# Kernel optimization log

Measured on AMD Instinct MI355X. Metric: run time of the kernel, lower is better.

The kernel has to match this reference:

```python
import jax, jax.numpy as jnp
import numpy as np
from jax.scipy.special import logsumexp

B, N, D, H = 8, 2048, 3, 256
BLUR = 0.001            # geomloss blur
EPS0 = 32.0             # ~diameter^2/2 for unit-std gaussian clouds
N_ITERS = 14            # eps-scaling steps down to blur^2
EPS_LIST = np.geomspace(EPS0, BLUR ** 2, N_ITERS).astype(np.float32)


def _sqdist(x, y):
    # x: [B,N,3], y: [B,M,3] -> [B,N,M] squared euclidean distance
    x2 = jnp.sum(x * x, -1)[:, :, None]
    y2 = jnp.sum(y * y, -1)[:, None, :]
    xy = jnp.einsum('bnd,bmd->bnm', x, y)
    return jnp.maximum(x2 + y2 - 2.0 * xy, 0.0)


def sinkhorn_potential_g(x, y):
    """Log-domain Sinkhorn (p=2 cost ||x-y||^2/2, uniform weights) with
    epsilon scaling; returns second dual potential g over y. Mimics
    geomloss.SamplesLoss('sinkhorn', p=2, blur=0.001, potentials=True)."""
    C = 0.5 * _sqdist(x, y)                      # [B,N,M]
    n, m = x.shape[1], y.shape[1]
    loga = -jnp.log(jnp.float32(n))
    logb = -jnp.log(jnp.float32(m))
    f = jnp.zeros((x.shape[0], n), C.dtype)
    g = jnp.zeros((x.shape[0], m), C.dtype)
    for eps in EPS_LIST:
        f = -eps * logsumexp(logb + (g[:, None, :] - C) / eps, axis=2)
        g = -eps * logsumexp(loga + (f[:, :, None] - C) / eps, axis=1)
    return g


def get_hard_assignment(x, y):
    # idx such that y[idx] is the OT match for x
    g = sinkhorn_potential_g(x, y)                       # [B,M]
    C_minus_g = _sqdist(x, y) - g[:, None, :]            # [B,N,M]
    return jnp.argmin(C_minus_g, axis=2)                 # [B,N]


def setup_inputs() -> dict:
    key = jax.random.key(0)
    ks = jax.random.split(key, 8)
    return {
        'cloud': jax.random.normal(ks[0], (B, N, D), jnp.float32),
        'noise': jax.random.normal(ks[1], (B, N, D), jnp.float32),
        't': jax.random.uniform(ks[2], (B,), jnp.float32),
        'W1': jax.random.normal(ks[3], (D, H), jnp.float32) * 0.1,
        'Wt': jax.random.normal(ks[4], (H,), jnp.float32) * 0.1,
        'b1': jnp.zeros((H,), jnp.float32),
        'W2': jax.random.normal(ks[5], (H, D), jnp.float32) * 0.1,
        'b2': jnp.zeros((D,), jnp.float32),
    }


def reference(cloud, noise, t, W1, Wt, b1, W2, b2):
    # std normalization (torch.std -> unbiased, ddof=1), done under no_grad
    std = jnp.std(cloud, axis=(1, 2), keepdims=True, ddof=1)
    x0 = cloud / std
    idx = get_hard_assignment(noise, x0)                 # [B,N] int
    x0_aligned = jnp.take_along_axis(x0, idx[:, :, None], axis=1)  # [B,N,3]
    tv = t[:, None, None]
    x_t = (1.0 - tv) * x0_aligned + tv * noise
    # stand-in diffusion network: per-point MLP conditioned on t
    h = jax.nn.relu(jnp.einsum('bnd,dh->bnh', x_t, W1) + tv * Wt + b1)
    v_pred = jnp.einsum('bnh,hd->bnd', h, W2) + b2
    v = noise - x0_aligned
    return v_pred, v
```

## Files before the change

### kernel.cpp

```cpp
#include <hip/hip_runtime.h>
#include <math.h>

#define B_ 8
#define N_ 2048
#define D_ 3
#define H_ 256
#define ND_ (N_*D_)
#define BN_ (B_*N_)

__global__ __launch_bounds__(256) void std_kernel(const float* __restrict__ cloud,
                                                  float* __restrict__ stdv) {
  __shared__ float red[256];
  int b = blockIdx.x, tid = threadIdx.x;
  const float* p = cloud + (size_t)b * ND_;
  float s = 0.f;
  for (int i = tid; i < ND_; i += 256) s += p[i];
  red[tid] = s; __syncthreads();
  for (int off = 128; off > 0; off >>= 1) {
    if (tid < off) red[tid] += red[tid + off];
    __syncthreads();
  }
  float mean = red[0] / (float)ND_;
  __syncthreads();
  float ss = 0.f;
  for (int i = tid; i < ND_; i += 256) { float d = p[i] - mean; ss += d * d; }
  red[tid] = ss; __syncthreads();
  for (int off = 128; off > 0; off >>= 1) {
    if (tid < off) red[tid] += red[tid + off];
    __syncthreads();
  }
  if (tid == 0) stdv[b] = sqrtf(red[0] / (float)(ND_ - 1));
}

__global__ __launch_bounds__(256) void prep_kernel(const float* __restrict__ cloud,
    const float* __restrict__ noise, const float* __restrict__ stdv,
    float4* __restrict__ x0p, float4* __restrict__ np4,
    float* __restrict__ f, float* __restrict__ g) {
  int i = blockIdx.x * 256 + threadIdx.x;
  if (i >= BN_) return;
  int b = i >> 11;
  float sd = stdv[b];
  float cx = cloud[3*i] / sd, cy = cloud[3*i+1] / sd, cz = cloud[3*i+2] / sd;
  x0p[i] = make_float4(cx, cy, cz, cx*cx + cy*cy + cz*cz);
  float ax = noise[3*i], ay = noise[3*i+1], az = noise[3*i+2];
  np4[i] = make_float4(ax, ay, az, ax*ax + ay*ay + az*az);
  f[i] = 0.f; g[i] = 0.f;
}

__global__ __launch_bounds__(256, 2) void lse_kernel(
    const float4* __restrict__ outer, const float4* __restrict__ inner,
    const float* __restrict__ pin, float* __restrict__ pout,
    float scl, float kk, float hh, float c1, float c2) {
  __shared__ float4 sP[N_];
  int tid = threadIdx.x;
  int b = blockIdx.x >> 7;
  int rowBase = (blockIdx.x & 127) << 4;
  int base = b * N_;
  for (int j = tid; j < N_; j += 256) {
    float4 p = inner[base + j];
    float q = kk * pin[base + j] - hh * p.w;
    sP[j] = make_float4(scl * p.x, scl * p.y, scl * p.z, q);
  }
  __syncthreads();
  int wave = tid >> 6, lane = tid & 63;
  int r0 = base + rowBase + (wave << 2);
  float4 A0 = outer[r0], A1 = outer[r0+1], A2 = outer[r0+2], A3 = outer[r0+3];
  float a0x = scl*A0.x, a0y = scl*A0.y, a0z = scl*A0.z, rc0 = -hh*A0.w;
  float a1x = scl*A1.x, a1y = scl*A1.y, a1z = scl*A1.z, rc1 = -hh*A1.w;
  float a2x = scl*A2.x, a2y = scl*A2.y, a2z = scl*A2.z, rc2 = -hh*A2.w;
  float a3x = scl*A3.x, a3y = scl*A3.y, a3z = scl*A3.z, rc3 = -hh*A3.w;
  float v0[32], v1[32], v2[32], v3[32];
  float m0 = -INFINITY, m1 = -INFINITY, m2 = -INFINITY, m3 = -INFINITY;
#pragma unroll
  for (int jj = 0; jj < 32; ++jj) {
    float4 p = sP[(jj << 6) + lane];
    float t0 = fmaf(p.x, a0x, p.w); t0 = fmaf(p.y, a0y, t0); t0 = fmaf(p.z, a0z, t0);
    v0[jj] = t0; m0 = fmaxf(m0, t0);
    float t1 = fmaf(p.x, a1x, p.w); t1 = fmaf(p.y, a1y, t1); t1 = fmaf(p.z, a1z, t1);
    v1[jj] = t1; m1 = fmaxf(m1, t1);
    float t2 = fmaf(p.x, a2x, p.w); t2 = fmaf(p.y, a2y, t2); t2 = fmaf(p.z, a2z, t2);
    v2[jj] = t2; m2 = fmaxf(m2, t2);
    float t3 = fmaf(p.x, a3x, p.w); t3 = fmaf(p.y, a3y, t3); t3 = fmaf(p.z, a3z, t3);
    v3[jj] = t3; m3 = fmaxf(m3, t3);
  }
#pragma unroll
  for (int off = 32; off >= 1; off >>= 1) {
    m0 = fmaxf(m0, __shfl_xor(m0, off, 64));
    m1 = fmaxf(m1, __shfl_xor(m1, off, 64));
    m2 = fmaxf(m2, __shfl_xor(m2, off, 64));
    m3 = fmaxf(m3, __shfl_xor(m3, off, 64));
  }
  float s0 = 0.f, s1 = 0.f, s2 = 0.f, s3 = 0.f;
#pragma unroll
  for (int jj = 0; jj < 32; ++jj) {
    s0 += __builtin_amdgcn_exp2f(v0[jj] - m0);
    s1 += __builtin_amdgcn_exp2f(v1[jj] - m1);
    s2 += __builtin_amdgcn_exp2f(v2[jj] - m2);
    s3 += __builtin_amdgcn_exp2f(v3[jj] - m3);
  }
#pragma unroll
  for (int off = 32; off >= 1; off >>= 1) {
    s0 += __shfl_xor(s0, off, 64);
    s1 += __shfl_xor(s1, off, 64);
    s2 += __shfl_xor(s2, off, 64);
    s3 += __shfl_xor(s3, off, 64);
  }
  if (lane == 0) {
    pout[r0]   = fmaf(c1, rc0 + m0 + __builtin_amdgcn_logf(s0), c2);
    pout[r0+1] = fmaf(c1, rc1 + m1 + __builtin_amdgcn_logf(s1), c2);
    pout[r0+2] = fmaf(c1, rc2 + m2 + __builtin_amdgcn_logf(s2), c2);
    pout[r0+3] = fmaf(c1, rc3 + m3 + __builtin_amdgcn_logf(s3), c2);
  }
}

__global__ __launch_bounds__(256) void assign_mlp_kernel(
    const float4* __restrict__ np4, const float4* __restrict__ x0p,
    const float* __restrict__ g, const float* __restrict__ t,
    const float* __restrict__ W1, const float* __restrict__ Wt,
    const float* __restrict__ b1, const float* __restrict__ W2,
    const float* __restrict__ b2, float* __restrict__ out) {
  __shared__ float4 sPts[N_];
  __shared__ float  sg[N_];
  __shared__ float  sW1[3*H_], sWt[H_], sb1[H_], sW2[H_*3], sb2[3];
  int tid = threadIdx.x;
  int b = blockIdx.x >> 8;
  int rowBase = (blockIdx.x & 255) << 3;
  int base = b * N_;
  for (int j = tid; j < N_; j += 256) { sPts[j] = x0p[base+j]; sg[j] = g[base+j]; }
  for (int i = tid; i < 3*H_; i += 256) { sW1[i] = W1[i]; sW2[i] = W2[i]; }
  if (tid < H_) { sWt[tid] = Wt[tid]; sb1[tid] = b1[tid]; }
  if (tid < 3) sb2[tid] = b2[tid];
  __syncthreads();
  int wave = tid >> 6, lane = tid & 63;
  float tb = t[b];
  for (int rr = 0; rr < 2; ++rr) {
    int r = rowBase + (wave << 1) + rr;
    float4 A = np4[base + r];
    float best = INFINITY; int bidx = 0;
#pragma unroll
    for (int jj = 0; jj < 32; ++jj) {
      int j = (jj << 6) + lane;
      float4 p = sPts[j];
      float d = A.x*p.x + A.y*p.y + A.z*p.z;
      float val = fmaxf(A.w + p.w - 2.0f*d, 0.0f) - sg[j];
      if (val < best) { best = val; bidx = j; }
    }
#pragma unroll
    for (int off = 32; off >= 1; off >>= 1) {
      float ov = __shfl_xor(best, off, 64);
      int   oi = __shfl_xor(bidx, off, 64);
      if (ov < best || (ov == best && oi < bidx)) { best = ov; bidx = oi; }
    }
    float4 xa = sPts[bidx];
    float xtx = (1.0f - tb)*xa.x + tb*A.x;
    float xty = (1.0f - tb)*xa.y + tb*A.y;
    float xtz = (1.0f - tb)*xa.z + tb*A.z;
    float acc0 = 0.f, acc1 = 0.f, acc2 = 0.f;
#pragma unroll
    for (int hh = 0; hh < 4; ++hh) {
      int h = (hh << 6) + lane;
      float hv = xtx*sW1[h] + xty*sW1[H_+h] + xtz*sW1[2*H_+h] + tb*sWt[h] + sb1[h];
      hv = fmaxf(hv, 0.0f);
      acc0 += hv * sW2[3*h];
      acc1 += hv * sW2[3*h+1];
      acc2 += hv * sW2[3*h+2];
    }
#pragma unroll
    for (int off = 32; off >= 1; off >>= 1) {
      acc0 += __shfl_xor(acc0, off, 64);
      acc1 += __shfl_xor(acc1, off, 64);
      acc2 += __shfl_xor(acc2, off, 64);
    }
    if (lane == 0) {
      int gi = base + r;
      out[3*gi]   = acc0 + sb2[0];
      out[3*gi+1] = acc1 + sb2[1];
      out[3*gi+2] = acc2 + sb2[2];
      out[3*BN_ + 3*gi]   = A.x - xa.x;
      out[3*BN_ + 3*gi+1] = A.y - xa.y;
      out[3*BN_ + 3*gi+2] = A.z - xa.z;
    }
  }
}

extern "C" void kernel_launch(void* const* d_in, const int* in_sizes, int n_in,
                              void* d_out, int out_size, void* d_ws, size_t ws_size,
                              hipStream_t stream) {
  (void)in_sizes; (void)n_in; (void)out_size; (void)ws_size;
  const float* cloud = (const float*)d_in[0];
  const float* noise = (const float*)d_in[1];
  const float* t     = (const float*)d_in[2];
  const float* W1    = (const float*)d_in[3];
  const float* Wt    = (const float*)d_in[4];
  const float* b1    = (const float*)d_in[5];
  const float* W2    = (const float*)d_in[6];
  const float* b2w   = (const float*)d_in[7];
  float* out = (float*)d_out;

  float* ws   = (float*)d_ws;
  float* stdv = ws;
  float4* x0p = (float4*)(ws + 16);
  float4* np4 = (float4*)(ws + 16 + 4*BN_);
  float* f    = ws + 16 + 8*BN_;
  float* g    = f + BN_;

  std_kernel<<<B_, 256, 0, stream>>>(cloud, stdv);
  prep_kernel<<<BN_/256, 256, 0, stream>>>(cloud, noise, stdv, x0p, np4, f, g);

  const double LOG2E = 1.4426950408889634074;
  const double LN2   = 0.6931471805599453094;
  const double logw  = -log(2048.0);
  const double l0 = log10(32.0), l1 = log10(1e-6);
  for (int kit = 0; kit < 14; ++kit) {
    double epsd = pow(10.0, l0 + (l1 - l0) * ((double)kit / 13.0));
    float eps = (float)epsd;
    float kk  = (float)(LOG2E / (double)eps);
    float hh  = 0.5f * kk;
    float scl = sqrtf(kk);
    float c1  = (float)(-(double)eps * LN2);
    float c2  = (float)(-(double)eps * logw);
    lse_kernel<<<B_*(N_/16), 256, 0, stream>>>(np4, x0p, g, f, scl, kk, hh, c1, c2);
    lse_kernel<<<B_*(N_/16), 256, 0, stream>>>(x0p, np4, f, g, scl, kk, hh, c1, c2);
  }

  assign_mlp_kernel<<<B_*(N_/8), 256, 0, stream>>>(np4, x0p, g, t, W1, Wt, b1, W2, b2w, out);
}
```

Baseline: 415.9 us.

## Fuse all Sinkhorn iterations into one persistent kernel with per-batch grid barriers

Replaces the 28 separate log-sum-exp launches with a single persistent kernel of 256 blocks (32 per batch). Blocks synchronise through atomic counter/generation barriers between half-iterations, and the per-iteration epsilon constants are passed in as a table. This removes launch overhead and inter-kernel gaps. In exchange each block handles 64 rows instead of 16, so there are fewer blocks than before, and correctness depends on all 256 blocks being co-resident on the device.

```diff
diff --git a/kernel.cpp b/kernel.cpp
--- a/kernel.cpp
+++ b/kernel.cpp
@@ -7,6 +7,11 @@
 #define H_ 256
 #define ND_ (N_*D_)
 #define BN_ (B_*N_)
+#define NITER_ 14
+
+struct EpsTab { float scl[NITER_], kk[NITER_], hh[NITER_], c1[NITER_], c2[NITER_]; };
+
+__device__ unsigned g_bar[256];
 
 __global__ __launch_bounds__(256) void std_kernel(const float* __restrict__ cloud,
                                                   float* __restrict__ stdv) {
@@ -37,6 +42,8 @@
     float4* __restrict__ x0p, float4* __restrict__ np4,
     float* __restrict__ f, float* __restrict__ g) {
   int i = blockIdx.x * 256 + threadIdx.x;
+  if (blockIdx.x == 0)
+    __hip_atomic_store(&g_bar[threadIdx.x], 0u, __ATOMIC_RELAXED, __HIP_MEMORY_SCOPE_AGENT);
   if (i >= BN_) return;
   int b = i >> 11;
   float sd = stdv[b];
@@ -47,69 +54,108 @@
   f[i] = 0.f; g[i] = 0.f;
 }
 
-__global__ __launch_bounds__(256, 2) void lse_kernel(
-    const float4* __restrict__ outer, const float4* __restrict__ inner,
-    const float* __restrict__ pin, float* __restrict__ pout,
-    float scl, float kk, float hh, float c1, float c2) {
+__device__ inline void batch_barrier(unsigned* cnt, unsigned* gen, unsigned epoch) {
+  __syncthreads();
+  if (threadIdx.x == 0) {
+    __threadfence();
+    unsigned old = __hip_atomic_fetch_add(cnt, 1u, __ATOMIC_ACQ_REL, __HIP_MEMORY_SCOPE_AGENT);
+    if (old == 31u) {
+      __hip_atomic_store(cnt, 0u, __ATOMIC_RELAXED, __HIP_MEMORY_SCOPE_AGENT);
+      __hip_atomic_fetch_add(gen, 1u, __ATOMIC_ACQ_REL, __HIP_MEMORY_SCOPE_AGENT);
+    } else {
+      while (__hip_atomic_load(gen, __ATOMIC_ACQUIRE, __HIP_MEMORY_SCOPE_AGENT) < epoch) {
+        __builtin_amdgcn_s_sleep(2);
+      }
+    }
+    __threadfence();
+  }
+  __syncthreads();
+}
+
+__global__ __launch_bounds__(256, 2) void sinkhorn_kernel(
+    const float4* __restrict__ x0p, const float4* __restrict__ np4,
+    float* f, float* g, EpsTab tab) {
   __shared__ float4 sP[N_];
   int tid = threadIdx.x;
-  int b = blockIdx.x >> 7;
-  int rowBase = (blockIdx.x & 127) << 4;
+  int b   = blockIdx.x >> 5;
+  int blk = blockIdx.x & 31;
   int base = b * N_;
-  for (int j = tid; j < N_; j += 256) {
-    float4 p = inner[base + j];
-    float q = kk * pin[base + j] - hh * p.w;
-    sP[j] = make_float4(scl * p.x, scl * p.y, scl * p.z, q);
-  }
-  __syncthreads();
+  unsigned* cnt = &g_bar[b * 16];
+  unsigned* gen = &g_bar[128 + b * 16];
   int wave = tid >> 6, lane = tid & 63;
-  int r0 = base + rowBase + (wave << 2);
-  float4 A0 = outer[r0], A1 = outer[r0+1], A2 = outer[r0+2], A3 = outer[r0+3];
-  float a0x = scl*A0.x, a0y = scl*A0.y, a0z = scl*A0.z, rc0 = -hh*A0.w;
-  float a1x = scl*A1.x, a1y = scl*A1.y, a1z = scl*A1.z, rc1 = -hh*A1.w;
-  float a2x = scl*A2.x, a2y = scl*A2.y, a2z = scl*A2.z, rc2 = -hh*A2.w;
-  float a3x = scl*A3.x, a3y = scl*A3.y, a3z = scl*A3.z, rc3 = -hh*A3.w;
-  float v0[32], v1[32], v2[32], v3[32];
-  float m0 = -INFINITY, m1 = -INFINITY, m2 = -INFINITY, m3 = -INFINITY;
-#pragma unroll
-  for (int jj = 0; jj < 32; ++jj) {
-    float4 p = sP[(jj << 6) + lane];
-    float t0 = fmaf(p.x, a0x, p.w); t0 = fmaf(p.y, a0y, t0); t0 = fmaf(p.z, a0z, t0);
-    v0[jj] = t0; m0 = fmaxf(m0, t0);
-    float t1 = fmaf(p.x, a1x, p.w); t1 = fmaf(p.y, a1y, t1); t1 = fmaf(p.z, a1z, t1);
-    v1[jj] = t1; m1 = fmaxf(m1, t1);
-    float t2 = fmaf(p.x, a2x, p.w); t2 = fmaf(p.y, a2y, t2); t2 = fmaf(p.z, a2z, t2);
-    v2[jj] = t2; m2 = fmaxf(m2, t2);
-    float t3 = fmaf(p.x, a3x, p.w); t3 = fmaf(p.y, a3y, t3); t3 = fmaf(p.z, a3z, t3);
-    v3[jj] = t3; m3 = fmaxf(m3, t3);
-  }
-#pragma unroll
-  for (int off = 32; off >= 1; off >>= 1) {
-    m0 = fmaxf(m0, __shfl_xor(m0, off, 64));
-    m1 = fmaxf(m1, __shfl_xor(m1, off, 64));
-    m2 = fmaxf(m2, __shfl_xor(m2, off, 64));
-    m3 = fmaxf(m3, __shfl_xor(m3, off, 64));
-  }
-  float s0 = 0.f, s1 = 0.f, s2 = 0.f, s3 = 0.f;
-#pragma unroll
-  for (int jj = 0; jj < 32; ++jj) {
-    s0 += __builtin_amdgcn_exp2f(v0[jj] - m0);
-    s1 += __builtin_amdgcn_exp2f(v1[jj] - m1);
-    s2 += __builtin_amdgcn_exp2f(v2[jj] - m2);
-    s3 += __builtin_amdgcn_exp2f(v3[jj] - m3);
-  }
-#pragma unroll
-  for (int off = 32; off >= 1; off >>= 1) {
-    s0 += __shfl_xor(s0, off, 64);
-    s1 += __shfl_xor(s1, off, 64);
-    s2 += __shfl_xor(s2, off, 64);
-    s3 += __shfl_xor(s3, off, 64);
-  }
-  if (lane == 0) {
-    pout[r0]   = fmaf(c1, rc0 + m0 + __builtin_amdgcn_logf(s0), c2);
-    pout[r0+1] = fmaf(c1, rc1 + m1 + __builtin_amdgcn_logf(s1), c2);
-    pout[r0+2] = fmaf(c1, rc2 + m2 + __builtin_amdgcn_logf(s2), c2);
-    pout[r0+3] = fmaf(c1, rc3 + m3 + __builtin_amdgcn_logf(s3), c2);
+  unsigned epoch = 0;
+  for (int kit = 0; kit < NITER_; ++kit) {
+    float scl = tab.scl[kit], kk = tab.kk[kit], hh = tab.hh[kit];
+    float c1 = tab.c1[kit], c2 = tab.c2[kit];
+    for (int half = 0; half < 2; ++half) {
+      const float4* outer = half ? x0p : np4;
+      const float4* inner = half ? np4 : x0p;
+      float*        pin   = half ? f : g;
+      float*        pout  = half ? g : f;
+      for (int j = tid; j < N_; j += 256) {
+        float4 p = inner[base + j];
+        float pot = __hip_atomic_load(&pin[base + j], __ATOMIC_RELAXED, __HIP_MEMORY_SCOPE_AGENT);
+        float q = fmaf(kk, pot, -hh * p.w);
+        sP[j] = make_float4(scl * p.x, scl * p.y, scl * p.z, q);
+      }
+      __syncthreads();
+      for (int grp = 0; grp < 4; ++grp) {
+        int r0 = base + (blk << 6) + (grp << 4) + (wave << 2);
+        float4 A0 = outer[r0], A1 = outer[r0+1], A2 = outer[r0+2], A3 = outer[r0+3];
+        float a0x = scl*A0.x, a0y = scl*A0.y, a0z = scl*A0.z, rc0 = -hh*A0.w;
+        float a1x = scl*A1.x, a1y = scl*A1.y, a1z = scl*A1.z, rc1 = -hh*A1.w;
+        float a2x = scl*A2.x, a2y = scl*A2.y, a2z = scl*A2.z, rc2 = -hh*A2.w;
+        float a3x = scl*A3.x, a3y = scl*A3.y, a3z = scl*A3.z, rc3 = -hh*A3.w;
+        float v0[32], v1[32], v2[32], v3[32];
+        float m0 = -INFINITY, m1 = -INFINITY, m2 = -INFINITY, m3 = -INFINITY;
+#pragma unroll
+        for (int jj = 0; jj < 32; ++jj) {
+          float4 p = sP[(jj << 6) + lane];
+          float t0 = fmaf(p.x, a0x, p.w); t0 = fmaf(p.y, a0y, t0); t0 = fmaf(p.z, a0z, t0);
+          v0[jj] = t0; m0 = fmaxf(m0, t0);
+          float t1 = fmaf(p.x, a1x, p.w); t1 = fmaf(p.y, a1y, t1); t1 = fmaf(p.z, a1z, t1);
+          v1[jj] = t1; m1 = fmaxf(m1, t1);
+          float t2 = fmaf(p.x, a2x, p.w); t2 = fmaf(p.y, a2y, t2); t2 = fmaf(p.z, a2z, t2);
+          v2[jj] = t2; m2 = fmaxf(m2, t2);
+          float t3 = fmaf(p.x, a3x, p.w); t3 = fmaf(p.y, a3y, t3); t3 = fmaf(p.z, a3z, t3);
+          v3[jj] = t3; m3 = fmaxf(m3, t3);
+        }
+#pragma unroll
+        for (int off = 32; off >= 1; off >>= 1) {
+          m0 = fmaxf(m0, __shfl_xor(m0, off, 64));
+          m1 = fmaxf(m1, __shfl_xor(m1, off, 64));
+          m2 = fmaxf(m2, __shfl_xor(m2, off, 64));
+          m3 = fmaxf(m3, __shfl_xor(m3, off, 64));
+        }
+        float s0 = 0.f, s1 = 0.f, s2 = 0.f, s3 = 0.f;
+#pragma unroll
+        for (int jj = 0; jj < 32; ++jj) {
+          s0 += __builtin_amdgcn_exp2f(v0[jj] - m0);
+          s1 += __builtin_amdgcn_exp2f(v1[jj] - m1);
+          s2 += __builtin_amdgcn_exp2f(v2[jj] - m2);
+          s3 += __builtin_amdgcn_exp2f(v3[jj] - m3);
+        }
+#pragma unroll
+        for (int off = 32; off >= 1; off >>= 1) {
+          s0 += __shfl_xor(s0, off, 64);
+          s1 += __shfl_xor(s1, off, 64);
+          s2 += __shfl_xor(s2, off, 64);
+          s3 += __shfl_xor(s3, off, 64);
+        }
+        if (lane == 0) {
+          float o0 = fmaf(c1, rc0 + m0 + __builtin_amdgcn_logf(s0), c2);
+          float o1 = fmaf(c1, rc1 + m1 + __builtin_amdgcn_logf(s1), c2);
+          float o2 = fmaf(c1, rc2 + m2 + __builtin_amdgcn_logf(s2), c2);
+          float o3 = fmaf(c1, rc3 + m3 + __builtin_amdgcn_logf(s3), c2);
+          __hip_atomic_store(&pout[r0],   o0, __ATOMIC_RELAXED, __HIP_MEMORY_SCOPE_AGENT);
+          __hip_atomic_store(&pout[r0+1], o1, __ATOMIC_RELAXED, __HIP_MEMORY_SCOPE_AGENT);
+          __hip_atomic_store(&pout[r0+2], o2, __ATOMIC_RELAXED, __HIP_MEMORY_SCOPE_AGENT);
+          __hip_atomic_store(&pout[r0+3], o3, __ATOMIC_RELAXED, __HIP_MEMORY_SCOPE_AGENT);
+        }
+      }
+      ++epoch;
+      batch_barrier(cnt, gen, epoch);
+    }
   }
 }
 
@@ -211,17 +257,18 @@
   const double LN2   = 0.6931471805599453094;
   const double logw  = -log(2048.0);
   const double l0 = log10(32.0), l1 = log10(1e-6);
-  for (int kit = 0; kit < 14; ++kit) {
+  EpsTab tab;
+  for (int kit = 0; kit < NITER_; ++kit) {
     double epsd = pow(10.0, l0 + (l1 - l0) * ((double)kit / 13.0));
     float eps = (float)epsd;
-    float kk  = (float)(LOG2E / (double)eps);
-    float hh  = 0.5f * kk;
-    float scl = sqrtf(kk);
-    float c1  = (float)(-(double)eps * LN2);
-    float c2  = (float)(-(double)eps * logw);
-    lse_kernel<<<B_*(N_/16), 256, 0, stream>>>(np4, x0p, g, f, scl, kk, hh, c1, c2);
-    lse_kernel<<<B_*(N_/16), 256, 0, stream>>>(x0p, np4, f, g, scl, kk, hh, c1, c2);
-  }
+    tab.kk[kit]  = (float)(LOG2E / (double)eps);
+    tab.hh[kit]  = 0.5f * tab.kk[kit];
+    tab.scl[kit] = sqrtf(tab.kk[kit]);
+    tab.c1[kit]  = (float)(-(double)eps * LN2);
+    tab.c2[kit]  = (float)(-(double)eps * logw);
+  }
+
+  sinkhorn_kernel<<<256, 256, 0, stream>>>(x0p, np4, f, g, tab);
 
   assign_mlp_kernel<<<B_*(N_/8), 256, 0, stream>>>(np4, x0p, g, t, W1, Wt, b1, W2, b2w, out);
 }
```

After: 1.049 ms. +152.2%, slower.
